# Optimization experiments

Hardware: AMD Instinct MI355X
Metric: run time of the kernel (lower is better)

Reference implementation:

```python
import jax, jax.numpy as jnp
import numpy as np

MIN_SIGMA = 0.1
MAX_SIGMA = 1.0
R = int(np.ceil(4.0 * MAX_SIGMA))  # max kernel radius -> 4
K = 2 * R + 1                      # static Kmax -> 9 (odd)


def setup_inputs() -> dict:
    key = jax.random.key(0)
    k1, k2 = jax.random.split(key)
    x1 = jax.random.normal(k1, (128, 3, 512, 512), dtype=jnp.float32)
    t = jax.random.uniform(k2, (128,), dtype=jnp.float32)
    return {"x1": x1, "t": t}


def _make_kernels(sigma):
    # sigma: [B]. Build per-sample normalized Gaussian kernels of effective
    # size k_i = 2*ceil(4*sigma_i)+1, zero-padded to the static KxK grid.
    coords = jnp.arange(K, dtype=jnp.float32) - (K // 2)
    y, x = jnp.meshgrid(coords, coords, indexing='ij')
    base = y * y + x * x                                   # [K,K]
    r = jnp.ceil(4.0 * sigma)                              # [B] per-sample radius
    within = jnp.abs(coords)[None, :] <= r[:, None]        # [B,K]
    mask = within[:, :, None] & within[:, None, :]         # [B,K,K]
    kern = jnp.exp(-base[None] / (2.0 * sigma * sigma)[:, None, None])
    kern = jnp.where(mask, kern, 0.0)
    return kern / jnp.sum(kern, axis=(1, 2), keepdims=True)


def reference(x1, t):
    B, C, H, W = x1.shape
    sigma = MIN_SIGMA + t * (MAX_SIGMA - MIN_SIGMA)        # get_sigma_t
    kern = _make_kernels(sigma)                            # [B,K,K]
    kern = jnp.repeat(kern, C, axis=0)[:, None]            # [B*C,1,K,K] depthwise
    x_ = x1.reshape(1, B * C, H, W)
    out = jax.lax.conv_general_dilated(
        x_, kern, window_strides=(1, 1), padding=[(R, R), (R, R)],
        feature_group_count=B * C,
        dimension_numbers=('NCHW', 'OIHW', 'NCHW'))
    x1_blurred = out.reshape(B, C, H, W)
    tb = t[:, None, None, None]
    # get_mu_t(x1, x1_blurred, t) = t*blurred + (1-t)*x1
    return tb * x1_blurred + (1.0 - tb) * x1
```

## Files before the change

### kernel.cpp

```cpp
#include <hip/hip_runtime.h>
#include <math.h>


#define TILE 64
#define HALO 4
#define KK 9
#define LW 72
#define IMG 512

__global__ __launch_bounds__(256) void blur_blend_kernel(
    const float* __restrict__ x, const float* __restrict__ t,
    float* __restrict__ out)
{
    __shared__ __align__(16) float s_in[LW][LW];
    __shared__ __align__(16) float s_tmp[LW][TILE];

    const int tid   = threadIdx.x;
    const int bx    = blockIdx.x;
    const int by    = blockIdx.y;
    const int plane = blockIdx.z;
    const int b     = plane / 3;

    const float tb     = t[b];
    const float sigma  = 0.1f + tb * 0.9f;
    const float r      = ceilf(4.0f * sigma);
    const float inv2s2 = 1.0f / (2.0f * sigma * sigma);
    float w[KK];
    float wsum = 0.0f;
#pragma unroll
    for (int k = 0; k < KK; ++k) {
        float d = (float)(k - HALO);
        float v = (fabsf(d) <= r) ? expf(-d * d * inv2s2) : 0.0f;
        w[k] = v;
        wsum += v;
    }
    const float winv = 1.0f / wsum;
#pragma unroll
    for (int k = 0; k < KK; ++k) w[k] *= winv;

    const float* plane_in  = x   + (size_t)plane * IMG * IMG;
    float*       plane_out = out + (size_t)plane * IMG * IMG;
    const int gx0 = bx * TILE - HALO;
    const int gy0 = by * TILE - HALO;

    for (int slot = tid; slot < LW * (LW / 4); slot += 256) {
        const int row = slot / (LW / 4);
        const int qc  = slot % (LW / 4);
        const int gy  = gy0 + row;
        const int gx  = gx0 + qc * 4;
        float4 v = make_float4(0.f, 0.f, 0.f, 0.f);
        if ((unsigned)gy < (unsigned)IMG) {
            if (gx >= 0 && gx + 3 < IMG) {
                v = *(const float4*)(plane_in + (size_t)gy * IMG + gx);
            } else {
                float* pv = &v.x;
#pragma unroll
                for (int j = 0; j < 4; ++j) {
                    const int g = gx + j;
                    if ((unsigned)g < (unsigned)IMG)
                        pv[j] = plane_in[(size_t)gy * IMG + g];
                }
            }
        }
        *(float4*)&s_in[row][qc * 4] = v;
    }
    __syncthreads();

    for (int slot = tid; slot < LW * (TILE / 4); slot += 256) {
        const int row = slot / (TILE / 4);
        const int qc  = slot % (TILE / 4);
        float f[12];
        *(float4*)&f[0] = *(const float4*)&s_in[row][qc * 4 + 0];
        *(float4*)&f[4] = *(const float4*)&s_in[row][qc * 4 + 4];
        *(float4*)&f[8] = *(const float4*)&s_in[row][qc * 4 + 8];
        float4 o;
        float* po = &o.x;
#pragma unroll
        for (int j = 0; j < 4; ++j) {
            float acc = 0.0f;
#pragma unroll
            for (int k = 0; k < KK; ++k) acc += w[k] * f[j + k];
            po[j] = acc;
        }
        *(float4*)&s_tmp[row][qc * 4] = o;
    }
    __syncthreads();

    const float one_m_t = 1.0f - tb;
    for (int slot = tid; slot < TILE * (TILE / 4); slot += 256) {
        const int row = slot / (TILE / 4);
        const int qc  = slot % (TILE / 4);
        float4 acc = make_float4(0.f, 0.f, 0.f, 0.f);
#pragma unroll
        for (int k = 0; k < KK; ++k) {
            const float4 v = *(const float4*)&s_tmp[row + k][qc * 4];
            acc.x += w[k] * v.x;
            acc.y += w[k] * v.y;
            acc.z += w[k] * v.z;
            acc.w += w[k] * v.w;
        }
        const float4 orig = *(const float4*)&s_in[row + HALO][qc * 4 + HALO];
        float4 res;
        res.x = tb * acc.x + one_m_t * orig.x;
        res.y = tb * acc.y + one_m_t * orig.y;
        res.z = tb * acc.z + one_m_t * orig.z;
        res.w = tb * acc.w + one_m_t * orig.w;
        const int gy = by * TILE + row;
        const int gx = bx * TILE + qc * 4;
        *(float4*)(plane_out + (size_t)gy * IMG + gx) = res;
    }
}

extern "C" void kernel_launch(void* const* d_in, const int* in_sizes, int n_in,
                              void* d_out, int out_size, void* d_ws, size_t ws_size,
                              hipStream_t stream) {
    const float* x = (const float*)d_in[0];
    const float* t = (const float*)d_in[1];
    float* out = (float*)d_out;
    dim3 grid(IMG / TILE, IMG / TILE, 128 * 3);
    blur_blend_kernel<<<grid, 256, 0, stream>>>(x, t, out);
}
```

Before: 677.3 us.

## Merge smem buffers, register-block horizontal and vertical passes, use nontemporal stores

Replaces the two shared arrays with one padded buffer (stride 76) that the horizontal pass overwrites in place. Each thread now computes 16 horizontal outputs from 24 loaded values, and 4 rows by 4 columns of vertical outputs from a sliding window of 12 rows. This cuts redundant shared-memory reads and halves LDS footprint, which may raise occupancy. Outputs are written with nontemporal stores so they bypass the cache. The costs are higher register pressure and an extra barrier for the in-place writeback.

```diff
diff --git a/kernel.cpp b/kernel.cpp
--- a/kernel.cpp
+++ b/kernel.cpp
@@ -6,14 +6,16 @@
 #define HALO 4
 #define KK 9
 #define LW 72
+#define LSTR 76
 #define IMG 512
+
+typedef float vfloat4 __attribute__((ext_vector_type(4)));
 
 __global__ __launch_bounds__(256) void blur_blend_kernel(
     const float* __restrict__ x, const float* __restrict__ t,
     float* __restrict__ out)
 {
-    __shared__ __align__(16) float s_in[LW][LW];
-    __shared__ __align__(16) float s_tmp[LW][TILE];
+    __shared__ __align__(16) float s[LW * LSTR];
 
     const int tid   = threadIdx.x;
     const int bx    = blockIdx.x;
@@ -23,14 +25,14 @@
 
     const float tb     = t[b];
     const float sigma  = 0.1f + tb * 0.9f;
-    const float r      = ceilf(4.0f * sigma);
+    const float rmax   = ceilf(4.0f * sigma);
     const float inv2s2 = 1.0f / (2.0f * sigma * sigma);
     float w[KK];
     float wsum = 0.0f;
 #pragma unroll
     for (int k = 0; k < KK; ++k) {
         float d = (float)(k - HALO);
-        float v = (fabsf(d) <= r) ? expf(-d * d * inv2s2) : 0.0f;
+        float v = (fabsf(d) <= rmax) ? expf(-d * d * inv2s2) : 0.0f;
         w[k] = v;
         wsum += v;
     }
@@ -38,14 +40,14 @@
 #pragma unroll
     for (int k = 0; k < KK; ++k) w[k] *= winv;
 
-    const float* plane_in  = x   + (size_t)plane * IMG * IMG;
-    float*       plane_out = out + (size_t)plane * IMG * IMG;
+    const float* plane_in  = x   + (size_t)plane * (IMG * IMG);
+    float*       plane_out = out + (size_t)plane * (IMG * IMG);
     const int gx0 = bx * TILE - HALO;
     const int gy0 = by * TILE - HALO;
 
     for (int slot = tid; slot < LW * (LW / 4); slot += 256) {
         const int row = slot / (LW / 4);
-        const int qc  = slot % (LW / 4);
+        const int qc  = slot - row * (LW / 4);
         const int gy  = gy0 + row;
         const int gx  = gx0 + qc * 4;
         float4 v = make_float4(0.f, 0.f, 0.f, 0.f);
@@ -62,52 +64,90 @@
                 }
             }
         }
-        *(float4*)&s_in[row][qc * 4] = v;
+        *(float4*)&s[row * LSTR + qc * 4] = v;
     }
     __syncthreads();
 
-    for (int slot = tid; slot < LW * (TILE / 4); slot += 256) {
-        const int row = slot / (TILE / 4);
-        const int qc  = slot % (TILE / 4);
-        float f[12];
-        *(float4*)&f[0] = *(const float4*)&s_in[row][qc * 4 + 0];
-        *(float4*)&f[4] = *(const float4*)&s_in[row][qc * 4 + 4];
-        *(float4*)&f[8] = *(const float4*)&s_in[row][qc * 4 + 8];
-        float4 o;
-        float* po = &o.x;
+    const int r0 = (tid >> 4) * 4;
+    const int qx = (tid & 15) * 4;
+    float4 orig[4];
 #pragma unroll
-        for (int j = 0; j < 4; ++j) {
+    for (int o = 0; o < 4; ++o)
+        orig[o] = *(const float4*)&s[(r0 + HALO + o) * LSTR + qx + HALO];
+
+    const int hrow0 = tid >> 2;
+    const int hc0   = (tid & 3) * 16;
+    float h0[16];
+    {
+        float f[24];
+#pragma unroll
+        for (int q = 0; q < 6; ++q)
+            *(float4*)&f[q * 4] = *(const float4*)&s[hrow0 * LSTR + hc0 + q * 4];
+#pragma unroll
+        for (int j = 0; j < 16; ++j) {
             float acc = 0.0f;
 #pragma unroll
             for (int k = 0; k < KK; ++k) acc += w[k] * f[j + k];
-            po[j] = acc;
+            h0[j] = acc;
         }
-        *(float4*)&s_tmp[row][qc * 4] = o;
+    }
+    const int hrow1 = (tid + 256) >> 2;
+    const int hc1   = ((tid + 256) & 3) * 16;
+    float h1[16];
+    if (tid < 32) {
+        float f[24];
+#pragma unroll
+        for (int q = 0; q < 6; ++q)
+            *(float4*)&f[q * 4] = *(const float4*)&s[hrow1 * LSTR + hc1 + q * 4];
+#pragma unroll
+        for (int j = 0; j < 16; ++j) {
+            float acc = 0.0f;
+#pragma unroll
+            for (int k = 0; k < KK; ++k) acc += w[k] * f[j + k];
+            h1[j] = acc;
+        }
     }
     __syncthreads();
 
+#pragma unroll
+    for (int q = 0; q < 4; ++q)
+        *(float4*)&s[hrow0 * LSTR + hc0 + HALO + q * 4] = *(const float4*)&h0[q * 4];
+    if (tid < 32) {
+#pragma unroll
+        for (int q = 0; q < 4; ++q)
+            *(float4*)&s[hrow1 * LSTR + hc1 + HALO + q * 4] = *(const float4*)&h1[q * 4];
+    }
+    __syncthreads();
+
+    float4 acc[4];
+#pragma unroll
+    for (int o = 0; o < 4; ++o) acc[o] = make_float4(0.f, 0.f, 0.f, 0.f);
+#pragma unroll
+    for (int rr = 0; rr < 12; ++rr) {
+        const float4 v = *(const float4*)&s[(r0 + rr) * LSTR + qx + HALO];
+#pragma unroll
+        for (int o = 0; o < 4; ++o) {
+            const int k = rr - o;
+            if (k >= 0 && k < KK) {
+                acc[o].x += w[k] * v.x;
+                acc[o].y += w[k] * v.y;
+                acc[o].z += w[k] * v.z;
+                acc[o].w += w[k] * v.w;
+            }
+        }
+    }
     const float one_m_t = 1.0f - tb;
-    for (int slot = tid; slot < TILE * (TILE / 4); slot += 256) {
-        const int row = slot / (TILE / 4);
-        const int qc  = slot % (TILE / 4);
-        float4 acc = make_float4(0.f, 0.f, 0.f, 0.f);
+    const int gxout = bx * TILE + qx;
 #pragma unroll
-        for (int k = 0; k < KK; ++k) {
-            const float4 v = *(const float4*)&s_tmp[row + k][qc * 4];
-            acc.x += w[k] * v.x;
-            acc.y += w[k] * v.y;
-            acc.z += w[k] * v.z;
-            acc.w += w[k] * v.w;
-        }
-        const float4 orig = *(const float4*)&s_in[row + HALO][qc * 4 + HALO];
-        float4 res;
-        res.x = tb * acc.x + one_m_t * orig.x;
-        res.y = tb * acc.y + one_m_t * orig.y;
-        res.z = tb * acc.z + one_m_t * orig.z;
-        res.w = tb * acc.w + one_m_t * orig.w;
-        const int gy = by * TILE + row;
-        const int gx = bx * TILE + qc * 4;
-        *(float4*)(plane_out + (size_t)gy * IMG + gx) = res;
+    for (int o = 0; o < 4; ++o) {
+        vfloat4 res;
+        res.x = tb * acc[o].x + one_m_t * orig[o].x;
+        res.y = tb * acc[o].y + one_m_t * orig[o].y;
+        res.z = tb * acc[o].z + one_m_t * orig[o].z;
+        res.w = tb * acc[o].w + one_m_t * orig[o].w;
+        const int gy = by * TILE + r0 + o;
+        __builtin_nontemporal_store(res,
+            (vfloat4*)(plane_out + (size_t)gy * IMG + gxout));
     }
 }
 
```

New measurement: 655.2 us. 1.03x faster.
